# Kernel optimization log

Measured on AMD Instinct MI355X. Metric: run time of the kernel, lower is better.

Reference implementation:

```python
import jax, jax.numpy as jnp
import numpy as np

GS = 256      # grid/node count
PARAM = 128   # feature width
KC = 32       # keepconst (constant features)
I1, I2 = 64, 32
PK = PARAM - KC
K_DIV = 16.0  # neighbor-count normalizer
EPS = 1e-3    # Keras BatchNorm default epsilon
B = 4


def _bn(x, g, b, m, v):
    # inference-mode batch norm over last axis
    return (x - m) * jax.lax.rsqrt(v + EPS) * g + b


def setup_inputs() -> dict:
    key = jax.random.key(0)
    ks = jax.random.split(key, 24)
    mat = (jax.random.uniform(ks[0], (B, GS, GS)) < (K_DIV / GS)).astype(jnp.float32)
    val = jax.random.normal(ks[1], (B, GS, PARAM), dtype=jnp.float32)
    def w(k, shape):
        fan = shape[0] if len(shape) > 1 else shape[0]
        return jax.random.normal(k, shape, dtype=jnp.float32) * (1.0 / np.sqrt(fan))
    inp = {
        'mat': mat, 'val': val,
        'M1': w(ks[2], (2 * PARAM, I1)), 'B1': 0.05 * jax.random.normal(ks[3], (I1,)),
        'M2': w(ks[4], (I1, I2)),        'B2': 0.05 * jax.random.normal(ks[5], (I2,)),
        'M3': w(ks[6], (I2, PK)),        'B3': 0.05 * jax.random.normal(ks[7], (PK,)),
    }
    for idx, d in zip((1, 2, 3), (I1, I2, PK)):
        kk = jax.random.split(ks[7 + idx], 4)
        inp[f'g{idx}'] = 1.0 + 0.1 * jax.random.normal(kk[0], (d,), dtype=jnp.float32)
        inp[f'b{idx}'] = 0.1 * jax.random.normal(kk[1], (d,), dtype=jnp.float32)
        inp[f'm{idx}'] = 0.1 * jax.random.normal(kk[2], (d,), dtype=jnp.float32)
        inp[f'v{idx}'] = jax.random.uniform(kk[3], (d,), dtype=jnp.float32, minval=0.5, maxval=1.5)
    return inp


def reference(mat, val, M1, B1, M2, B2, M3, B3,
              g1, b1, m1, v1, g2, b2, m2, v2, g3, b3, m3, v3):
    con = val[:, :, :KC]
    # selector matmuls == gather: pair i -> (a=i//GS, b=i%GS)
    feat = jnp.repeat(val, GS, axis=1)          # (B, GS*GS, PARAM) = val_a
    vb = jnp.tile(val, (1, GS, 1))              # (B, GS*GS, PARAM) = val_b
    premlp = jnp.concatenate([feat, vb - feat], axis=-1)  # (B, GS*GS, 2*PARAM)
    s = jax.nn.relu(_bn(premlp @ M1 + B1, g1, b1, m1, v1))
    s = jax.nn.relu(_bn(s @ M2 + B2, g2, b2, m2, v2))
    s = jax.nn.relu(_bn(s @ M3 + B3, g3, b3, m3, v3))      # (B, GS*GS, PK)
    res = s.reshape(val.shape[0], GS, GS, PK)               # (B, a, b, PK)
    # masked scatter-sum over neighbor axis b
    summ = jnp.einsum('babk,bab->bak'.replace('a', 'x').replace('b', 'y', 1), res, mat) if False else \
        jnp.einsum('bxyk,bxy->bxk', res, mat)               # (B, GS, PK)
    var = jnp.clip(summ / K_DIV, -1.0, 1.0)                 # advrelu([-1,1]) == clip
    return jnp.concatenate([con, var], axis=-1)             # (B, GS, PARAM)
```

## Files before the change

kernel.cpp:

```cpp
#include <hip/hip_runtime.h>

#define GS    256
#define PARAM 128
#define KC    32
#define I1    64
#define I2    32
#define PK    96
#define B_    4
#define NROWS (B_ * GS)
#define EPS   1e-3f
#define KDIV_INV (1.0f / 16.0f)
#define CHUNK 32

constexpr int U_OFF   = 0;
constexpr int W_OFF   = NROWS * I1;
constexpr int M2F_OFF = 2 * NROWS * I1;
constexpr int C2_OFF  = M2F_OFF + I1 * I2;
constexpr int M3F_OFF = C2_OFF + I2;
constexpr int C3_OFF  = M3F_OFF + I2 * PK;
constexpr int C1_OFF  = C3_OFF + PK;

__global__ __launch_bounds__(256) void glmlp_precompute(
    const float* __restrict__ val, const float* __restrict__ M1,
    const float* __restrict__ B1,
    const float* __restrict__ M2, const float* __restrict__ B2,
    const float* __restrict__ M3, const float* __restrict__ B3,
    const float* __restrict__ g1, const float* __restrict__ b1,
    const float* __restrict__ m1, const float* __restrict__ v1,
    const float* __restrict__ g2, const float* __restrict__ b2,
    const float* __restrict__ m2, const float* __restrict__ v2,
    const float* __restrict__ g3, const float* __restrict__ b3,
    const float* __restrict__ m3, const float* __restrict__ v3,
    float* __restrict__ ws, float* __restrict__ out)
{
    const int blk = blockIdx.x;
    const int t = threadIdx.x;

    if (blk < NROWS) {
        __shared__ float vrow[PARAM];
        __shared__ float red[4][I1];
        const int r = blk;
        if (t < PARAM) vrow[t] = val[r * PARAM + t];
        __syncthreads();

        if (t < KC) out[r * PARAM + t] = vrow[t];

        const int i = t & (I1 - 1);
        const int q = t >> 6;
        const float* __restrict__ Mb = M1 + ((q >> 1) ? (PARAM * I1) : 0);
        const int p0 = (q & 1) * 64;
        float acc = 0.f;
        #pragma unroll 8
        for (int p = 0; p < 64; ++p)
            acc = fmaf(vrow[p0 + p], Mb[(p0 + p) * I1 + i], acc);
        red[q][i] = acc;
        __syncthreads();

        if (q == 0) {
            const float T  = red[0][i] + red[1][i];
            const float Wv = red[2][i] + red[3][i];
            const float s1 = g1[i] * rsqrtf(v1[i] + EPS);
            ws[U_OFF + r * I1 + i] = (T - Wv) * s1;
            ws[W_OFF + r * I1 + i] = Wv * s1;
        }
    } else {
        if (t < I1) {
            const float s1 = g1[t] * rsqrtf(v1[t] + EPS);
            ws[C1_OFF + t] = B1[t] * s1 + b1[t] - m1[t] * s1;
        }
        if (t < I2) {
            const float s2 = g2[t] * rsqrtf(v2[t] + EPS);
            ws[C2_OFF + t] = B2[t] * s2 + b2[t] - m2[t] * s2;
        }
        if (t < PK) {
            const float s3 = g3[t] * rsqrtf(v3[t] + EPS);
            ws[C3_OFF + t] = B3[t] * s3 + b3[t] - m3[t] * s3;
        }
        for (int idx = t; idx < I1 * I2; idx += 256) {
            const int j = idx & (I2 - 1);
            const float s2 = g2[j] * rsqrtf(v2[j] + EPS);
            ws[M2F_OFF + idx] = M2[idx] * s2;
        }
        for (int idx = t; idx < I2 * PK; idx += 256) {
            const int k = idx % PK;
            const float s3 = g3[k] * rsqrtf(v3[k] + EPS);
            ws[M3F_OFF + idx] = M3[idx] * s3;
        }
    }
}

__global__ __launch_bounds__(256) void glmlp_pairs(
    const float* __restrict__ mat, const float* __restrict__ ws,
    float* __restrict__ out)
{
    __shared__ float m2s[I1 * I2];
    __shared__ float m3s[I2 * PK];
    __shared__ float uxs[I1];
    __shared__ float c2s[I2];
    __shared__ float c3s[PK];
    __shared__ float H1[CHUNK][I1];
    __shared__ float H2[CHUNK][I2];
    __shared__ int   acty[GS];
    __shared__ float partial[2][PK];
    __shared__ int   cnt;

    const int r = blockIdx.x;
    const int t = threadIdx.x;
    const int wbase = r & ~(GS - 1);
    const float* __restrict__ W = ws + W_OFF;

    if (t == 0) cnt = 0;
    const float mv = mat[r * GS + t];
    for (int idx = t; idx < I1 * I2; idx += 256) m2s[idx] = ws[M2F_OFF + idx];
    for (int idx = t; idx < I2 * PK; idx += 256) m3s[idx] = ws[M3F_OFF + idx];
    if (t < I2) c2s[t] = ws[C2_OFF + t];
    if (t < PK) c3s[t] = ws[C3_OFF + t];
    if (t < I1) uxs[t] = ws[U_OFF + r * I1 + t] + ws[C1_OFF + t];
    __syncthreads();

    if (mv != 0.0f) acty[atomicAdd(&cnt, 1)] = t;
    __syncthreads();
    const int n = cnt;

    const bool l3 = (t < 2 * PK);
    const int k = t % PK;
    const int h = t / PK;
    float accO = 0.0f;

    for (int base = 0; base < n; base += CHUNK) {
        const int nc = min(CHUNK, n - base);

        for (int idx = t; idx < nc * I1; idx += 256) {
            const int p = idx >> 6, i = idx & (I1 - 1);
            const int y = acty[base + p];
            H1[p][i] = fmaxf(uxs[i] + W[(wbase + y) * I1 + i], 0.0f);
        }
        __syncthreads();

        for (int idx = t; idx < nc * I2; idx += 256) {
            const int p = idx >> 5, j = idx & (I2 - 1);
            float a = c2s[j];
            const float4* h1p4 = (const float4*)&H1[p][0];
            #pragma unroll
            for (int i4 = 0; i4 < I1 / 4; ++i4) {
                const float4 hv = h1p4[i4];
                const int i = i4 * 4;
                a = fmaf(hv.x, m2s[(i + 0) * I2 + j], a);
                a = fmaf(hv.y, m2s[(i + 1) * I2 + j], a);
                a = fmaf(hv.z, m2s[(i + 2) * I2 + j], a);
                a = fmaf(hv.w, m2s[(i + 3) * I2 + j], a);
            }
            H2[p][j] = fmaxf(a, 0.0f);
        }
        __syncthreads();

        if (l3) {
            int p = h;
            for (; p + 2 < nc; p += 4) {
                float a0 = c3s[k], a1 = c3s[k];
                const float4* A4 = (const float4*)&H2[p][0];
                const float4* B4 = (const float4*)&H2[p + 2][0];
                #pragma unroll
                for (int i4 = 0; i4 < I2 / 4; ++i4) {
                    const float4 ha = A4[i4];
                    const float4 hb = B4[i4];
                    const int i = i4 * 4;
                    const float w0 = m3s[(i + 0) * PK + k];
                    const float w1 = m3s[(i + 1) * PK + k];
                    const float w2 = m3s[(i + 2) * PK + k];
                    const float w3 = m3s[(i + 3) * PK + k];
                    a0 = fmaf(ha.x, w0, a0);
                    a1 = fmaf(hb.x, w0, a1);
                    a0 = fmaf(ha.y, w1, a0);
                    a1 = fmaf(hb.y, w1, a1);
                    a0 = fmaf(ha.z, w2, a0);
                    a1 = fmaf(hb.z, w2, a1);
                    a0 = fmaf(ha.w, w3, a0);
                    a1 = fmaf(hb.w, w3, a1);
                }
                accO += fmaxf(a0, 0.0f) + fmaxf(a1, 0.0f);
            }
            for (; p < nc; p += 2) {
                float a0 = c3s[k];
                const float4* A4 = (const float4*)&H2[p][0];
                #pragma unroll
                for (int i4 = 0; i4 < I2 / 4; ++i4) {
                    const float4 ha = A4[i4];
                    const int i = i4 * 4;
                    a0 = fmaf(ha.x, m3s[(i + 0) * PK + k], a0);
                    a0 = fmaf(ha.y, m3s[(i + 1) * PK + k], a0);
                    a0 = fmaf(ha.z, m3s[(i + 2) * PK + k], a0);
                    a0 = fmaf(ha.w, m3s[(i + 3) * PK + k], a0);
                }
                accO += fmaxf(a0, 0.0f);
            }
        }
    }

    if (l3) partial[h][k] = accO;
    __syncthreads();

    if (t < PK) {
        float v = (partial[0][t] + partial[1][t]) * KDIV_INV;
        v = fminf(fmaxf(v, -1.0f), 1.0f);
        out[r * PARAM + KC + t] = v;
    }
}

extern "C" void kernel_launch(void* const* d_in, const int* in_sizes, int n_in,
                              void* d_out, int out_size, void* d_ws, size_t ws_size,
                              hipStream_t stream) {
    const float* mat = (const float*)d_in[0];
    const float* val = (const float*)d_in[1];
    const float* M1  = (const float*)d_in[2];
    const float* B1  = (const float*)d_in[3];
    const float* M2  = (const float*)d_in[4];
    const float* B2  = (const float*)d_in[5];
    const float* M3  = (const float*)d_in[6];
    const float* B3  = (const float*)d_in[7];
    const float* g1  = (const float*)d_in[8];
    const float* b1  = (const float*)d_in[9];
    const float* m1  = (const float*)d_in[10];
    const float* v1  = (const float*)d_in[11];
    const float* g2  = (const float*)d_in[12];
    const float* b2  = (const float*)d_in[13];
    const float* m2  = (const float*)d_in[14];
    const float* v2  = (const float*)d_in[15];
    const float* g3  = (const float*)d_in[16];
    const float* b3  = (const float*)d_in[17];
    const float* m3  = (const float*)d_in[18];
    const float* v3  = (const float*)d_in[19];

    float* ws  = (float*)d_ws;
    float* out = (float*)d_out;

    hipLaunchKernelGGL(glmlp_precompute, dim3(NROWS + 1), dim3(256), 0, stream,
                       val, M1, B1, M2, B2, M3, B3,
                       g1, b1, m1, v1, g2, b2, m2, v2, g3, b3, m3, v3,
                       ws, out);

    hipLaunchKernelGGL(glmlp_pairs, dim3(NROWS), dim3(256), 0, stream,
                       mat, ws, out);
}
```

Baseline: 129.1 us.

## Process one neighbor per wavefront using shuffles instead of shared-memory chunk staging

Replaces the chunked shared-memory staging of H1/H2 (with block-wide barriers between layers) with a per-wavefront pipeline. Each of the 4 waves handles one active neighbor at a time, keeps hidden activations in registers and broadcasts them with __shfl, and prefetches the next neighbor's W row. This removes the __syncthreads and LDS round trips per chunk. In exchange it adds many cross-lane shuffles, duplicates half of the layer-2 work across the two half-waves, and leaves lanes 32-63 computing redundant values for the layer-3 second half. It also splits FMA accumulators into pairs in the precompute and layer loops to shorten dependency chains.

New measurement: 122.7 us. 5.0% less time.

```diff
diff --git a/kernel.cpp b/kernel.cpp
--- a/kernel.cpp
+++ b/kernel.cpp
@@ -10,7 +10,6 @@
 #define NROWS (B_ * GS)
 #define EPS   1e-3f
 #define KDIV_INV (1.0f / 16.0f)
-#define CHUNK 32
 
 constexpr int U_OFF   = 0;
 constexpr int W_OFF   = NROWS * I1;
@@ -41,19 +40,20 @@
         __shared__ float red[4][I1];
         const int r = blk;
         if (t < PARAM) vrow[t] = val[r * PARAM + t];
+        if (t < KC) out[r * PARAM + t] = val[r * PARAM + t];
         __syncthreads();
-
-        if (t < KC) out[r * PARAM + t] = vrow[t];
 
         const int i = t & (I1 - 1);
         const int q = t >> 6;
         const float* __restrict__ Mb = M1 + ((q >> 1) ? (PARAM * I1) : 0);
         const int p0 = (q & 1) * 64;
-        float acc = 0.f;
+        float aa = 0.f, bb = 0.f;
         #pragma unroll 8
-        for (int p = 0; p < 64; ++p)
-            acc = fmaf(vrow[p0 + p], Mb[(p0 + p) * I1 + i], acc);
-        red[q][i] = acc;
+        for (int p = 0; p < 64; p += 2) {
+            aa = fmaf(vrow[p0 + p],     Mb[(p0 + p) * I1 + i],     aa);
+            bb = fmaf(vrow[p0 + p + 1], Mb[(p0 + p + 1) * I1 + i], bb);
+        }
+        red[q][i] = aa + bb;
         __syncthreads();
 
         if (q == 0) {
@@ -98,14 +98,16 @@
     __shared__ float uxs[I1];
     __shared__ float c2s[I2];
     __shared__ float c3s[PK];
-    __shared__ float H1[CHUNK][I1];
-    __shared__ float H2[CHUNK][I2];
+    __shared__ float partial[4][PK];
     __shared__ int   acty[GS];
-    __shared__ float partial[2][PK];
     __shared__ int   cnt;
 
     const int r = blockIdx.x;
     const int t = threadIdx.x;
+    const int lane = t & 63;
+    const int w = t >> 6;
+    const int jj = lane & 31;
+    const int p0 = (lane >> 5) * 32;
     const int wbase = r & ~(GS - 1);
     const float* __restrict__ W = ws + W_OFF;
 
@@ -122,86 +124,54 @@
     __syncthreads();
     const int n = cnt;
 
-    const bool l3 = (t < 2 * PK);
-    const int k = t % PK;
-    const int h = t / PK;
-    float accO = 0.0f;
-
-    for (int base = 0; base < n; base += CHUNK) {
-        const int nc = min(CHUNK, n - base);
-
-        for (int idx = t; idx < nc * I1; idx += 256) {
-            const int p = idx >> 6, i = idx & (I1 - 1);
-            const int y = acty[base + p];
-            H1[p][i] = fmaxf(uxs[i] + W[(wbase + y) * I1 + i], 0.0f);
-        }
-        __syncthreads();
-
-        for (int idx = t; idx < nc * I2; idx += 256) {
-            const int p = idx >> 5, j = idx & (I2 - 1);
-            float a = c2s[j];
-            const float4* h1p4 = (const float4*)&H1[p][0];
-            #pragma unroll
-            for (int i4 = 0; i4 < I1 / 4; ++i4) {
-                const float4 hv = h1p4[i4];
-                const int i = i4 * 4;
-                a = fmaf(hv.x, m2s[(i + 0) * I2 + j], a);
-                a = fmaf(hv.y, m2s[(i + 1) * I2 + j], a);
-                a = fmaf(hv.z, m2s[(i + 2) * I2 + j], a);
-                a = fmaf(hv.w, m2s[(i + 3) * I2 + j], a);
-            }
-            H2[p][j] = fmaxf(a, 0.0f);
-        }
-        __syncthreads();
-
-        if (l3) {
-            int p = h;
-            for (; p + 2 < nc; p += 4) {
-                float a0 = c3s[k], a1 = c3s[k];
-                const float4* A4 = (const float4*)&H2[p][0];
-                const float4* B4 = (const float4*)&H2[p + 2][0];
-                #pragma unroll
-                for (int i4 = 0; i4 < I2 / 4; ++i4) {
-                    const float4 ha = A4[i4];
-                    const float4 hb = B4[i4];
-                    const int i = i4 * 4;
-                    const float w0 = m3s[(i + 0) * PK + k];
-                    const float w1 = m3s[(i + 1) * PK + k];
-                    const float w2 = m3s[(i + 2) * PK + k];
-                    const float w3 = m3s[(i + 3) * PK + k];
-                    a0 = fmaf(ha.x, w0, a0);
-                    a1 = fmaf(hb.x, w0, a1);
-                    a0 = fmaf(ha.y, w1, a0);
-                    a1 = fmaf(hb.y, w1, a1);
-                    a0 = fmaf(ha.z, w2, a0);
-                    a1 = fmaf(hb.z, w2, a1);
-                    a0 = fmaf(ha.w, w3, a0);
-                    a1 = fmaf(hb.w, w3, a1);
-                }
-                accO += fmaxf(a0, 0.0f) + fmaxf(a1, 0.0f);
-            }
-            for (; p < nc; p += 2) {
-                float a0 = c3s[k];
-                const float4* A4 = (const float4*)&H2[p][0];
-                #pragma unroll
-                for (int i4 = 0; i4 < I2 / 4; ++i4) {
-                    const float4 ha = A4[i4];
-                    const int i = i4 * 4;
-                    a0 = fmaf(ha.x, m3s[(i + 0) * PK + k], a0);
-                    a0 = fmaf(ha.y, m3s[(i + 1) * PK + k], a0);
-                    a0 = fmaf(ha.z, m3s[(i + 2) * PK + k], a0);
-                    a0 = fmaf(ha.w, m3s[(i + 3) * PK + k], a0);
-                }
-                accO += fmaxf(a0, 0.0f);
-            }
-        }
+    const float ux   = uxs[lane];
+    const float c2j  = c2s[jj];
+    const float c3_0 = c3s[lane];
+    const float c3_1 = c3s[64 + jj];
+
+    float acc0 = 0.f, acc1 = 0.f;
+
+    int p = w;
+    float wv = (p < n) ? W[(wbase + acty[p]) * I1 + lane] : 0.f;
+    while (p < n) {
+        const int pn = p + 4;
+        const float wvn = (pn < n) ? W[(wbase + acty[pn]) * I1 + lane] : 0.f;
+
+        const float h1 = fmaxf(ux + wv, 0.f);
+
+        float a = 0.f, b = 0.f;
+        #pragma unroll
+        for (int s = 0; s < 32; s += 2) {
+            a = fmaf(__shfl(h1, p0 + s),     m2s[(p0 + s) * I2 + jj],     a);
+            b = fmaf(__shfl(h1, p0 + s + 1), m2s[(p0 + s + 1) * I2 + jj], b);
+        }
+        const float ab = a + b;
+        const float h2 = fmaxf(__shfl(ab, jj) + __shfl(ab, 32 + jj) + c2j, 0.f);
+
+        float d0a = c3_0, d0b = 0.f, d1a = c3_1, d1b = 0.f;
+        #pragma unroll
+        for (int i = 0; i < I2; i += 2) {
+            const float he = __shfl(h2, i);
+            const float ho = __shfl(h2, i + 1);
+            d0a = fmaf(he, m3s[i * PK + lane], d0a);
+            d0b = fmaf(ho, m3s[(i + 1) * PK + lane], d0b);
+            d1a = fmaf(he, m3s[i * PK + 64 + jj], d1a);
+            d1b = fmaf(ho, m3s[(i + 1) * PK + 64 + jj], d1b);
+        }
+        acc0 += fmaxf(d0a + d0b, 0.f);
+        acc1 += fmaxf(d1a + d1b, 0.f);
+
+        wv = wvn;
+        p = pn;
     }
 
-    if (l3) partial[h][k] = accO;
+    partial[w][lane] = acc0;
+    if (lane < 32) partial[w][64 + lane] = acc1;
     __syncthreads();
 
     if (t < PK) {
-        float v = (partial[0][t] + partial[1][t]) * KDIV_INV;
+        float v = (partial[0][t] + partial[1][t] + partial[2][t] + partial[3][t])
+                  * KDIV_INV;
         v = fminf(fmaxf(v, -1.0f), 1.0f);
         out[r * PARAM + KC + t] = v;
     }
```
